# Performance work log

Measured on AMD Instinct MI355X. Metric: run time of the kernel, lower is better.

The kernel has to match this reference:

```python
import jax, jax.numpy as jnp
import numpy as np

QMAX = 127.0

def _sym_quantize(t):
    # per-tensor symmetric int8 fake-quant: returns (quantized values as float, scale)
    scale = jnp.max(jnp.abs(t)) / QMAX
    q = jnp.clip(jnp.round(t / scale), -QMAX, QMAX)
    return q, scale

def setup_inputs() -> dict:
    key = jax.random.key(0)
    k1, k2, k3 = jax.random.split(key, 3)
    TOKENS, IN_F, OUT_F = 4096, 4096, 4096
    x = jax.random.normal(k1, (TOKENS, IN_F), dtype=jnp.float32)
    # int8-valued weight buffer (stored int32 for portability), symmetric range
    quantized_weight = jax.random.randint(k2, (OUT_F, IN_F), -127, 128, dtype=jnp.int32)
    weight_scale = jnp.float32(0.01)  # scalar per-tensor weight scale buffer
    bias = jax.random.normal(k3, (OUT_F,), dtype=jnp.float32)
    return {"x": x, "quantized_weight": quantized_weight,
            "weight_scale": weight_scale, "bias": bias}

def reference(x, quantized_weight, weight_scale, bias):
    q_x, x_scale = _sym_quantize(x)                      # [T, In] fake-quant activations
    w = quantized_weight.astype(jnp.float32)             # [Out, In]
    out = jnp.matmul(q_x, w.T)                           # fp32 GEMM on int8-valued operands
    out = out * (x_scale * weight_scale)                 # dequant scaling
    out = out + bias
    return out
```

## Files before the change

kernel.cpp:

```cpp
#include <hip/hip_runtime.h>

typedef __attribute__((ext_vector_type(4))) int int4v;

__device__ __forceinline__ void async_ld16(const void* g, void* l) {
  __builtin_amdgcn_global_load_lds(
      (const __attribute__((address_space(1))) void*)g,
      (__attribute__((address_space(3))) void*)l,
      16, 0, 0);
}

__global__ void absmax_kernel(const float* __restrict__ x,
                              unsigned int* __restrict__ out_bits, int n4) {
  const float4* x4 = (const float4*)x;
  float m = 0.0f;
  for (int i = blockIdx.x * blockDim.x + threadIdx.x; i < n4;
       i += gridDim.x * blockDim.x) {
    float4 v = x4[i];
    m = fmaxf(m, fabsf(v.x));
    m = fmaxf(m, fabsf(v.y));
    m = fmaxf(m, fabsf(v.z));
    m = fmaxf(m, fabsf(v.w));
  }
#pragma unroll
  for (int off = 32; off > 0; off >>= 1)
    m = fmaxf(m, __shfl_down(m, off, 64));
  __shared__ float wmax[4];
  const int wid = threadIdx.x >> 6;
  if ((threadIdx.x & 63) == 0) wmax[wid] = m;
  __syncthreads();
  if (threadIdx.x == 0) {
    float bm = fmaxf(fmaxf(wmax[0], wmax[1]), fmaxf(wmax[2], wmax[3]));
    atomicMax(out_bits, __float_as_uint(bm));
  }
}

__global__ void quant_x_kernel(const float* __restrict__ x,
                               const unsigned int* __restrict__ max_bits,
                               int* __restrict__ qx, int n4) {
  const float scale = __uint_as_float(*max_bits) / 127.0f;
  int i = blockIdx.x * blockDim.x + threadIdx.x;
  if (i >= n4) return;
  float4 v = ((const float4*)x)[i];
  int q0 = (int)fminf(fmaxf(rintf(v.x / scale), -127.0f), 127.0f);
  int q1 = (int)fminf(fmaxf(rintf(v.y / scale), -127.0f), 127.0f);
  int q2 = (int)fminf(fmaxf(rintf(v.z / scale), -127.0f), 127.0f);
  int q3 = (int)fminf(fmaxf(rintf(v.w / scale), -127.0f), 127.0f);
  unsigned int p = (unsigned int)(q0 & 255) | ((unsigned int)(q1 & 255) << 8) |
                   ((unsigned int)(q2 & 255) << 16) |
                   ((unsigned int)(q3 & 255) << 24);
  qx[i] = (int)p;
}

__global__ void pack_w_kernel(const int* __restrict__ w,
                              int* __restrict__ qw, int n4) {
  int i = blockIdx.x * blockDim.x + threadIdx.x;
  if (i >= n4) return;
  int4 v = ((const int4*)w)[i];
  unsigned int p = (unsigned int)(v.x & 255) | ((unsigned int)(v.y & 255) << 8) |
                   ((unsigned int)(v.z & 255) << 16) |
                   ((unsigned int)(v.w & 255) << 24);
  qw[i] = (int)p;
}

__global__ __launch_bounds__(256) void gemm_i8_kernel(
    const signed char* __restrict__ A,
    const signed char* __restrict__ B,
    const float* __restrict__ bias,
    const unsigned int* __restrict__ max_bits,
    const float* __restrict__ wscale,
    float* __restrict__ out, int K, int N) {
  __shared__ signed char As[128 * 64];
  __shared__ signed char Bs[128 * 64];

  const int tid = threadIdx.x;
  const int lane = tid & 63;
  const int wid = tid >> 6;
  const int row0 = blockIdx.y * 128;
  const int col0 = blockIdx.x * 128;
  const int wm = (wid >> 1) * 64;
  const int wn = (wid & 1) * 64;

  int4v acc[4][4] = {};

  signed char* lA = As + wid * 2048;
  signed char* lB = Bs + wid * 2048;
  const signed char* gA =
      A + (long)(row0 + wid * 32 + (lane >> 2)) * K + (lane & 3) * 16;
  const signed char* gB =
      B + (long)(col0 + wid * 32 + (lane >> 2)) * K + (lane & 3) * 16;

  const int fa = (wm + (lane & 15)) * 64 + (lane >> 4) * 16;
  const int fb = (wn + (lane & 15)) * 64 + (lane >> 4) * 16;

  for (int k0 = 0; k0 < K; k0 += 64) {
    __syncthreads();
    async_ld16(gA, lA);
    async_ld16(gA + 16 * (long)K, lA + 1024);
    async_ld16(gB, lB);
    async_ld16(gB + 16 * (long)K, lB + 1024);
    gA += 64;
    gB += 64;
    asm volatile("s_waitcnt vmcnt(0)" ::: "memory");
    __syncthreads();

    int4v a[4], b[4];
#pragma unroll
    for (int i = 0; i < 4; i++) {
      a[i] = *(const int4v*)(As + fa + i * 16 * 64);
      b[i] = *(const int4v*)(Bs + fb + i * 16 * 64);
    }
#pragma unroll
    for (int i = 0; i < 4; i++)
#pragma unroll
      for (int j = 0; j < 4; j++)
        acc[i][j] =
            __builtin_amdgcn_mfma_i32_16x16x64_i8(a[i], b[j], acc[i][j], 0, 0, 0);
  }

  const float s = (__uint_as_float(*max_bits) / 127.0f) * wscale[0];
  const int orow = row0 + wm + ((lane >> 4) << 2);
  const int ocol0 = col0 + wn + (lane & 15);
#pragma unroll
  for (int j = 0; j < 4; j++) {
    const int c = ocol0 + j * 16;
    const float bv = bias[c];
#pragma unroll
    for (int i = 0; i < 4; i++) {
#pragma unroll
      for (int r = 0; r < 4; r++) {
        out[(long)(orow + i * 16 + r) * N + c] = (float)acc[i][j][r] * s + bv;
      }
    }
  }
}

extern "C" void kernel_launch(void* const* d_in, const int* in_sizes, int n_in,
                              void* d_out, int out_size, void* d_ws,
                              size_t ws_size, hipStream_t stream) {
  const float* x = (const float*)d_in[0];
  const int* w = (const int*)d_in[1];
  const float* wscale = (const float*)d_in[2];
  const float* bias = (const float*)d_in[3];
  float* out = (float*)d_out;

  const int OUT_F = in_sizes[3];
  const int IN_F = in_sizes[1] / OUT_F;
  const int TOKENS = in_sizes[0] / IN_F;

  unsigned int* max_bits = (unsigned int*)d_ws;
  signed char* qx = (signed char*)d_ws + 256;
  signed char* qw = qx + (size_t)TOKENS * IN_F;

  hipMemsetAsync(d_ws, 0, 256, stream);

  const int nx4 = TOKENS * IN_F / 4;
  absmax_kernel<<<1024, 256, 0, stream>>>(x, max_bits, nx4);
  quant_x_kernel<<<(nx4 + 255) / 256, 256, 0, stream>>>(x, max_bits, (int*)qx,
                                                        nx4);
  const int nw4 = OUT_F * IN_F / 4;
  pack_w_kernel<<<(nw4 + 255) / 256, 256, 0, stream>>>(w, (int*)qw, nw4);

  dim3 grid(OUT_F / 128, TOKENS / 128);
  gemm_i8_kernel<<<grid, 256, 0, stream>>>(qx, qw, bias, max_bits, wscale, out,
                                           IN_F, OUT_F);
}
```

Baseline: 293.8 us.

## Swizzle LDS tiles in int8 GEMM and fuse quantize/pack kernels

Applies an XOR swizzle to the 16-byte K chunks when staging A/B tiles into LDS and when reading MFMA fragments, to reduce LDS bank conflicts. Replaces the atomicMax absmax plus memset with per-block partial maxima that every block of a single fused quant+pack kernel re-reduces. Weight packing and activation quantization now run in one launch. Each quant block redundantly reads 1024 partials, adding some global traffic.

```diff
diff --git a/kernel.cpp b/kernel.cpp
--- a/kernel.cpp
+++ b/kernel.cpp
@@ -1,6 +1,8 @@
 #include <hip/hip_runtime.h>
 
 typedef __attribute__((ext_vector_type(4))) int int4v;
+
+#define NB_MAX 1024
 
 __device__ __forceinline__ void async_ld16(const void* g, void* l) {
   __builtin_amdgcn_global_load_lds(
@@ -9,8 +11,8 @@
       16, 0, 0);
 }
 
-__global__ void absmax_kernel(const float* __restrict__ x,
-                              unsigned int* __restrict__ out_bits, int n4) {
+__global__ void absmax_partial_kernel(const float* __restrict__ x,
+                                      float* __restrict__ partial, int n4) {
   const float4* x4 = (const float4*)x;
   float m = 0.0f;
   for (int i = blockIdx.x * blockDim.x + threadIdx.x; i < n4;
@@ -28,45 +30,65 @@
   const int wid = threadIdx.x >> 6;
   if ((threadIdx.x & 63) == 0) wmax[wid] = m;
   __syncthreads();
-  if (threadIdx.x == 0) {
-    float bm = fmaxf(fmaxf(wmax[0], wmax[1]), fmaxf(wmax[2], wmax[3]));
-    atomicMax(out_bits, __float_as_uint(bm));
-  }
+  if (threadIdx.x == 0)
+    partial[blockIdx.x] =
+        fmaxf(fmaxf(wmax[0], wmax[1]), fmaxf(wmax[2], wmax[3]));
 }
 
-__global__ void quant_x_kernel(const float* __restrict__ x,
-                               const unsigned int* __restrict__ max_bits,
-                               int* __restrict__ qx, int n4) {
-  const float scale = __uint_as_float(*max_bits) / 127.0f;
-  int i = blockIdx.x * blockDim.x + threadIdx.x;
-  if (i >= n4) return;
-  float4 v = ((const float4*)x)[i];
-  int q0 = (int)fminf(fmaxf(rintf(v.x / scale), -127.0f), 127.0f);
-  int q1 = (int)fminf(fmaxf(rintf(v.y / scale), -127.0f), 127.0f);
-  int q2 = (int)fminf(fmaxf(rintf(v.z / scale), -127.0f), 127.0f);
-  int q3 = (int)fminf(fmaxf(rintf(v.w / scale), -127.0f), 127.0f);
-  unsigned int p = (unsigned int)(q0 & 255) | ((unsigned int)(q1 & 255) << 8) |
-                   ((unsigned int)(q2 & 255) << 16) |
-                   ((unsigned int)(q3 & 255) << 24);
-  qx[i] = (int)p;
+__device__ __forceinline__ float reduce_partials(const float* partial) {
+  __shared__ float smax;
+  float m = 0.0f;
+  for (int i = threadIdx.x; i < NB_MAX; i += blockDim.x)
+    m = fmaxf(m, partial[i]);
+#pragma unroll
+  for (int off = 32; off > 0; off >>= 1)
+    m = fmaxf(m, __shfl_down(m, off, 64));
+  __shared__ float wmax[4];
+  const int wid = threadIdx.x >> 6;
+  if ((threadIdx.x & 63) == 0) wmax[wid] = m;
+  __syncthreads();
+  if (threadIdx.x == 0)
+    smax = fmaxf(fmaxf(wmax[0], wmax[1]), fmaxf(wmax[2], wmax[3]));
+  __syncthreads();
+  return smax;
 }
 
-__global__ void pack_w_kernel(const int* __restrict__ w,
-                              int* __restrict__ qw, int n4) {
-  int i = blockIdx.x * blockDim.x + threadIdx.x;
-  if (i >= n4) return;
-  int4 v = ((const int4*)w)[i];
-  unsigned int p = (unsigned int)(v.x & 255) | ((unsigned int)(v.y & 255) << 8) |
-                   ((unsigned int)(v.z & 255) << 16) |
-                   ((unsigned int)(v.w & 255) << 24);
-  qw[i] = (int)p;
+__global__ void quant_pack_kernel(const float* __restrict__ x,
+                                  const int* __restrict__ w,
+                                  const float* __restrict__ partial,
+                                  float* __restrict__ scale_slot,
+                                  int* __restrict__ qx, int* __restrict__ qw,
+                                  int nx4, int nw4) {
+  const float scale = reduce_partials(partial) / 127.0f;
+  const int i = blockIdx.x * blockDim.x + threadIdx.x;
+  if (i == 0) *scale_slot = scale;
+  if (i < nx4) {
+    float4 v = ((const float4*)x)[i];
+    int q0 = (int)fminf(fmaxf(rintf(v.x / scale), -127.0f), 127.0f);
+    int q1 = (int)fminf(fmaxf(rintf(v.y / scale), -127.0f), 127.0f);
+    int q2 = (int)fminf(fmaxf(rintf(v.z / scale), -127.0f), 127.0f);
+    int q3 = (int)fminf(fmaxf(rintf(v.w / scale), -127.0f), 127.0f);
+    unsigned int p = (unsigned int)(q0 & 255) |
+                     ((unsigned int)(q1 & 255) << 8) |
+                     ((unsigned int)(q2 & 255) << 16) |
+                     ((unsigned int)(q3 & 255) << 24);
+    qx[i] = (int)p;
+  }
+  if (i < nw4) {
+    int4 v = ((const int4*)w)[i];
+    unsigned int p = (unsigned int)(v.x & 255) |
+                     ((unsigned int)(v.y & 255) << 8) |
+                     ((unsigned int)(v.z & 255) << 16) |
+                     ((unsigned int)(v.w & 255) << 24);
+    qw[i] = (int)p;
+  }
 }
 
 __global__ __launch_bounds__(256) void gemm_i8_kernel(
     const signed char* __restrict__ A,
     const signed char* __restrict__ B,
     const float* __restrict__ bias,
-    const unsigned int* __restrict__ max_bits,
+    const float* __restrict__ scale_slot,
     const float* __restrict__ wscale,
     float* __restrict__ out, int K, int N) {
   __shared__ signed char As[128 * 64];
@@ -84,13 +106,15 @@
 
   signed char* lA = As + wid * 2048;
   signed char* lB = Bs + wid * 2048;
+  const int kb_s = ((lane & 3) ^ ((lane >> 3) & 3)) * 16;
   const signed char* gA =
-      A + (long)(row0 + wid * 32 + (lane >> 2)) * K + (lane & 3) * 16;
+      A + (long)(row0 + wid * 32 + (lane >> 2)) * K + kb_s;
   const signed char* gB =
-      B + (long)(col0 + wid * 32 + (lane >> 2)) * K + (lane & 3) * 16;
+      B + (long)(col0 + wid * 32 + (lane >> 2)) * K + kb_s;
 
-  const int fa = (wm + (lane & 15)) * 64 + (lane >> 4) * 16;
-  const int fb = (wn + (lane & 15)) * 64 + (lane >> 4) * 16;
+  const int swz_f = (lane >> 1) & 3;
+  const int fa = (wm + (lane & 15)) * 64 + (((lane >> 4) ^ swz_f) << 4);
+  const int fb = (wn + (lane & 15)) * 64 + (((lane >> 4) ^ swz_f) << 4);
 
   for (int k0 = 0; k0 < K; k0 += 64) {
     __syncthreads();
@@ -117,7 +141,7 @@
             __builtin_amdgcn_mfma_i32_16x16x64_i8(a[i], b[j], acc[i][j], 0, 0, 0);
   }
 
-  const float s = (__uint_as_float(*max_bits) / 127.0f) * wscale[0];
+  const float s = scale_slot[0] * wscale[0];
   const int orow = row0 + wm + ((lane >> 4) << 2);
   const int ocol0 = col0 + wn + (lane & 15);
 #pragma unroll
@@ -147,20 +171,21 @@
   const int IN_F = in_sizes[1] / OUT_F;
   const int TOKENS = in_sizes[0] / IN_F;
 
-  unsigned int* max_bits = (unsigned int*)d_ws;
-  signed char* qx = (signed char*)d_ws + 256;
+  float* partial = (float*)d_ws;
+  float* scale_slot = partial + NB_MAX;
+  signed char* qx = (signed char*)d_ws + 8192;
   signed char* qw = qx + (size_t)TOKENS * IN_F;
 
-  hipMemsetAsync(d_ws, 0, 256, stream);
+  const int nx4 = TOKENS * IN_F / 4;
+  const int nw4 = OUT_F * IN_F / 4;
 
-  const int nx4 = TOKENS * IN_F / 4;
-  absmax_kernel<<<1024, 256, 0, stream>>>(x, max_bits, nx4);
-  quant_x_kernel<<<(nx4 + 255) / 256, 256, 0, stream>>>(x, max_bits, (int*)qx,
-                                                        nx4);
-  const int nw4 = OUT_F * IN_F / 4;
-  pack_w_kernel<<<(nw4 + 255) / 256, 256, 0, stream>>>(w, (int*)qw, nw4);
+  absmax_partial_kernel<<<NB_MAX, 256, 0, stream>>>(x, partial, nx4);
+
+  const int nmax = nx4 > nw4 ? nx4 : nw4;
+  quant_pack_kernel<<<(nmax + 255) / 256, 256, 0, stream>>>(
+      x, w, partial, scale_slot, (int*)qx, (int*)qw, nx4, nw4);
 
   dim3 grid(OUT_F / 128, TOKENS / 128);
-  gemm_i8_kernel<<<grid, 256, 0, stream>>>(qx, qw, bias, max_bits, wscale, out,
-                                           IN_F, OUT_F);
+  gemm_i8_kernel<<<grid, 256, 0, stream>>>(qx, qw, bias, scale_slot, wscale,
+                                           out, IN_F, OUT_F);
 }
```

Result: faster. 284.8 us (-3.1%).
